# Optimization experiments

Measured on AMD Instinct MI355X. Metric: run time of the kernel, lower is better.

## Reference

```python
import jax, jax.numpy as jnp
import numpy as np

ANNEAL = 0.01
N, D, NUM_CLASSES = 384, 128, 24


def setup_inputs() -> dict:
    key = jax.random.key(0)
    k1, k2 = jax.random.split(key)
    preds = jax.random.normal(k1, (N, D), dtype=jnp.float32)
    # L2-normalize embeddings (standard for SmoothAP cosine similarities)
    preds = preds / jnp.linalg.norm(preds, axis=1, keepdims=True)
    labels = jax.random.randint(k2, (N,), 0, NUM_CLASSES, dtype=jnp.int64)
    return {"preds": preds, "labels": labels}


def reference(preds, labels):
    n = preds.shape[0]
    dt = preds.dtype
    eye = jnp.eye(n, dtype=dt)
    # I_pos[i,j] = 1 iff same label and i != j (lmu.get_all_pairs_indices)
    I_pos = (labels[:, None] == labels[None, :]).astype(dt) * (1 - eye)
    sim = preds @ preds.T                              # [N, N]
    # sim_diff[a,b,c] = sim[a,c] - sim[a,b]  (unsqueeze(1) - unsqueeze(2))
    diff = sim[:, None, :] - sim[:, :, None]           # [N, N, N]
    sg = jax.nn.sigmoid(jnp.clip(diff / ANNEAL, -50.0, 50.0))
    sg = sg * (1 - eye)                                # zero where b == c
    # sum_c sg[a,b,c] * I_pos[a,c], then gate by I_pos[a,b]
    pos_sum = jnp.einsum('abc,ac->ab', sg, I_pos) * I_pos
    sim_pos_rk = 1 + I_pos + pos_sum                   # [N, N]
    sim_all_rk = 1 + jnp.sum(sg, axis=-1)              # [N, N]
    n_pos = jnp.sum(I_pos, axis=1) + 1                 # [N]
    per_i = jnp.sum(sim_pos_rk / sim_all_rk, axis=1) / n_pos
    ap = jnp.sum(jnp.where(n_pos > 1, per_i, jnp.zeros((), dt))) / n
    return (1 - ap)[None]                              # shape (1,), like torch
```

## Files before the change

### kernel.cpp

```cpp
#include <hip/hip_runtime.h>

#define N 384
#define NT 768
#define HALF_ITERS 96

__device__ const float KLOG2E = 144.26950408889634f;

__global__ __launch_bounds__(NT) void smoothap_fused(const float* __restrict__ preds,
                                                     const int* __restrict__ labels,
                                                     float* __restrict__ out) {
    __shared__ __align__(16) float4 s_pa[32];
    __shared__ __align__(16) float2 s_sp[N];
    __shared__ __align__(16) float2 s_part[N];
    __shared__ int   s_lab[N];
    __shared__ float s_red[24];

    const int a = blockIdx.x;
    const int t = threadIdx.x;
    const int half = (t >= N) ? 1 : 0;
    const int b = t - half * N;

    if (t < N) s_lab[t] = labels[t];
    if (t < 32) s_pa[t] = ((const float4*)(preds + (size_t)a * 128))[t];
    __syncthreads();

    if (t < N) {
        const float4* pt = (const float4*)(preds + (size_t)t * 128);
        float acc = 0.f;
#pragma unroll
        for (int k = 0; k < 32; ++k) {
            float4 v = pt[k];
            float4 w = s_pa[k];
            acc = fmaf(v.x, w.x, acc);
            acc = fmaf(v.y, w.y, acc);
            acc = fmaf(v.z, w.z, acc);
            acc = fmaf(v.w, w.w, acc);
        }
        const float posf = (s_lab[t] == s_lab[a] && t != a) ? 1.f : 0.f;
        s_sp[t] = make_float2(acc, posf);
    }
    __syncthreads();

    const float2 me = s_sp[b];
    const float mab = me.x * KLOG2E;
    const float posf = me.y;

    float all_sum = 0.f, pos_sum = 0.f;
    const float4* sp4 = (const float4*)s_sp;
    const int j0 = half * HALF_ITERS;
#pragma unroll 4
    for (int j = j0; j < j0 + HALF_ITERS; ++j) {
        float4 q = sp4[j];
        float e0 = fmaf(q.x, -KLOG2E, mab);
        float sg0 = __builtin_amdgcn_rcpf(1.f + __builtin_amdgcn_exp2f(e0));
        float e1 = fmaf(q.z, -KLOG2E, mab);
        float sg1 = __builtin_amdgcn_rcpf(1.f + __builtin_amdgcn_exp2f(e1));
        all_sum += sg0 + sg1;
        pos_sum = fmaf(sg0, q.y, pos_sum);
        pos_sum = fmaf(sg1, q.w, pos_sum);
    }
    if (half) s_part[b] = make_float2(all_sum, pos_sum);
    __syncthreads();

    float r = 0.f, np = 0.f;
    if (t < N) {
        const float2 o = s_part[b];
        const float all = all_sum + o.x - 0.5f;
        const float pos = pos_sum + o.y - 0.5f * posf;
        r = fmaf(posf, 1.f + pos, 1.f) / (1.f + all);
        np = posf;
    }

    const int lane = t & 63;
    const int wid = t >> 6;
#pragma unroll
    for (int off = 32; off; off >>= 1) {
        r += __shfl_down(r, off);
        np += __shfl_down(np, off);
    }
    if (lane == 0) {
        s_red[wid] = r;
        s_red[12 + wid] = np;
    }
    __syncthreads();
    if (t == 0) {
        float rs = 0.f, ns = 0.f;
#pragma unroll
        for (int w = 0; w < 12; ++w) {
            rs += s_red[w];
            ns += s_red[12 + w];
        }
        const float per_i = (ns > 0.5f) ? rs / (ns + 1.f) : 0.f;
        const float contrib = fmaf(per_i, -1.f / (float)N, (a == 0) ? 1.f : 0.f);
        atomicAdd(out, contrib);
    }
}

extern "C" void kernel_launch(void* const* d_in, const int* in_sizes, int n_in,
                              void* d_out, int out_size, void* d_ws, size_t ws_size,
                              hipStream_t stream) {
    const float* preds = (const float*)d_in[0];
    const int* labels = (const int*)d_in[1];
    float* out = (float*)d_out;

    hipMemsetAsync(out, 0, sizeof(float), stream);
    smoothap_fused<<<N, NT, 0, stream>>>(preds, labels, out);
}
```

Before: 82.74 us.

## Split each anchor row across two blocks of 384 threads

The grid changes from one 768-thread block per anchor to two 384-thread blocks per anchor. Each block handles half of the b indices, and each b is still split over two c-halves inside the block. The point is more, smaller blocks for better scheduling across CUs. The cost is that each anchor's full similarity row (the 384x128 dot products) is now computed twice, and the number of atomic adds doubles.

```diff
diff --git a/kernel.cpp b/kernel.cpp
--- a/kernel.cpp
+++ b/kernel.cpp
@@ -1,8 +1,9 @@
 #include <hip/hip_runtime.h>
 
 #define N 384
-#define NT 768
-#define HALF_ITERS 96
+#define NT 384
+#define HB 192
+#define HJ 96
 
 __device__ const float KLOG2E = 144.26950408889634f;
 
@@ -11,20 +12,19 @@
                                                      float* __restrict__ out) {
     __shared__ __align__(16) float4 s_pa[32];
     __shared__ __align__(16) float2 s_sp[N];
-    __shared__ __align__(16) float2 s_part[N];
+    __shared__ __align__(16) float2 s_part[HB];
     __shared__ int   s_lab[N];
-    __shared__ float s_red[24];
+    __shared__ float s_red[12];
 
-    const int a = blockIdx.x;
+    const int a = blockIdx.x >> 1;
+    const int bh = blockIdx.x & 1;
     const int t = threadIdx.x;
-    const int half = (t >= N) ? 1 : 0;
-    const int b = t - half * N;
 
-    if (t < N) s_lab[t] = labels[t];
+    s_lab[t] = labels[t];
     if (t < 32) s_pa[t] = ((const float4*)(preds + (size_t)a * 128))[t];
     __syncthreads();
 
-    if (t < N) {
+    {
         const float4* pt = (const float4*)(preds + (size_t)t * 128);
         float acc = 0.f;
 #pragma unroll
@@ -36,20 +36,24 @@
             acc = fmaf(v.z, w.z, acc);
             acc = fmaf(v.w, w.w, acc);
         }
-        const float posf = (s_lab[t] == s_lab[a] && t != a) ? 1.f : 0.f;
-        s_sp[t] = make_float2(acc, posf);
+        const float pf = (s_lab[t] == s_lab[a] && t != a) ? 1.f : 0.f;
+        s_sp[t] = make_float2(acc, pf);
     }
     __syncthreads();
 
-    const float2 me = s_sp[b];
-    const float mab = me.x * KLOG2E;
-    const float posf = me.y;
+    const int chalf = (t >= HB) ? 1 : 0;
+    const int b_local = t - chalf * HB;
+    const int b = bh * HB + b_local;
+    const float2 mb = s_sp[b];
+    const float mab = mb.x * KLOG2E;
+    const float posf = mb.y;
+    const float np = s_sp[t].y;
 
     float all_sum = 0.f, pos_sum = 0.f;
     const float4* sp4 = (const float4*)s_sp;
-    const int j0 = half * HALF_ITERS;
+    const int j0 = chalf * HJ;
 #pragma unroll 4
-    for (int j = j0; j < j0 + HALF_ITERS; ++j) {
+    for (int j = j0; j < j0 + HJ; ++j) {
         float4 q = sp4[j];
         float e0 = fmaf(q.x, -KLOG2E, mab);
         float sg0 = __builtin_amdgcn_rcpf(1.f + __builtin_amdgcn_exp2f(e0));
@@ -59,39 +63,39 @@
         pos_sum = fmaf(sg0, q.y, pos_sum);
         pos_sum = fmaf(sg1, q.w, pos_sum);
     }
-    if (half) s_part[b] = make_float2(all_sum, pos_sum);
+    if (chalf) s_part[b_local] = make_float2(all_sum, pos_sum);
     __syncthreads();
 
-    float r = 0.f, np = 0.f;
-    if (t < N) {
-        const float2 o = s_part[b];
+    float r = 0.f;
+    if (t < HB) {
+        const float2 o = s_part[b_local];
         const float all = all_sum + o.x - 0.5f;
         const float pos = pos_sum + o.y - 0.5f * posf;
         r = fmaf(posf, 1.f + pos, 1.f) / (1.f + all);
-        np = posf;
     }
 
     const int lane = t & 63;
     const int wid = t >> 6;
+    float rr = r, nn = np;
 #pragma unroll
     for (int off = 32; off; off >>= 1) {
-        r += __shfl_down(r, off);
-        np += __shfl_down(np, off);
+        rr += __shfl_down(rr, off);
+        nn += __shfl_down(nn, off);
     }
     if (lane == 0) {
-        s_red[wid] = r;
-        s_red[12 + wid] = np;
+        s_red[wid] = rr;
+        s_red[6 + wid] = nn;
     }
     __syncthreads();
     if (t == 0) {
         float rs = 0.f, ns = 0.f;
 #pragma unroll
-        for (int w = 0; w < 12; ++w) {
+        for (int w = 0; w < 6; ++w) {
             rs += s_red[w];
-            ns += s_red[12 + w];
+            ns += s_red[6 + w];
         }
-        const float per_i = (ns > 0.5f) ? rs / (ns + 1.f) : 0.f;
-        const float contrib = fmaf(per_i, -1.f / (float)N, (a == 0) ? 1.f : 0.f);
+        float contrib = (ns > 0.5f) ? -rs / ((ns + 1.f) * (float)N) : 0.f;
+        if (blockIdx.x == 0) contrib += 1.f;
         atomicAdd(out, contrib);
     }
 }
@@ -104,5 +108,5 @@
     float* out = (float*)d_out;
 
     hipMemsetAsync(out, 0, sizeof(float), stream);
-    smoothap_fused<<<N, NT, 0, stream>>>(preds, labels, out);
+    smoothap_fused<<<2 * N, NT, 0, stream>>>(preds, labels, out);
 }
```

After: 87.19 us. 5.4% more time.

## Factor sigmoid into per-element exponentials and compact positives to drop per-pair exp

Applied to the files above, without the earlier changes.

The sigmoid of a scaled similarity difference is rewritten as 1/(1 + A_b*E_c), where A = exp2(k*sim) and E = exp2(-k*sim) are computed once per element. This removes the per-pair exp from the inner loop and leaves one FMA plus one reciprocal per pair. The E values are also compacted with a ballot/popcount prefix so positives come first, which lets the positive sum drop its per-pair multiply and be accumulated only over the leading range. The clamp on each exponent bounds the products, but it differs from clamping the difference itself and could change accuracy for extreme similarities.

```diff
diff --git a/kernel.cpp b/kernel.cpp
--- a/kernel.cpp
+++ b/kernel.cpp
@@ -2,96 +2,141 @@
 
 #define N 384
 #define NT 768
-#define HALF_ITERS 96
+#define HJ 48
 
 __device__ const float KLOG2E = 144.26950408889634f;
+__device__ const float CL = 63.0f;
 
 __global__ __launch_bounds__(NT) void smoothap_fused(const float* __restrict__ preds,
                                                      const int* __restrict__ labels,
                                                      float* __restrict__ out) {
     __shared__ __align__(16) float4 s_pa[32];
-    __shared__ __align__(16) float2 s_sp[N];
+    __shared__ __align__(16) float2 s_AP[N];
+    __shared__ __align__(16) float  s_E[N];
     __shared__ __align__(16) float2 s_part[N];
-    __shared__ int   s_lab[N];
-    __shared__ float s_red[24];
+    __shared__ int   s_wpos[6];
+    __shared__ float s_red[12];
+    __shared__ int   s_P;
 
     const int a = blockIdx.x;
     const int t = threadIdx.x;
-    const int half = (t >= N) ? 1 : 0;
-    const int b = t - half * N;
+    const int lane = t & 63;
+    const int wid = t >> 6;
 
-    if (t < N) s_lab[t] = labels[t];
     if (t < 32) s_pa[t] = ((const float4*)(preds + (size_t)a * 128))[t];
     __syncthreads();
 
+    float posf_t = 0.f, E_t = 0.f;
     if (t < N) {
         const float4* pt = (const float4*)(preds + (size_t)t * 128);
-        float acc = 0.f;
+        float acc0 = 0.f, acc1 = 0.f;
 #pragma unroll
-        for (int k = 0; k < 32; ++k) {
-            float4 v = pt[k];
-            float4 w = s_pa[k];
-            acc = fmaf(v.x, w.x, acc);
-            acc = fmaf(v.y, w.y, acc);
-            acc = fmaf(v.z, w.z, acc);
-            acc = fmaf(v.w, w.w, acc);
+        for (int k = 0; k < 32; k += 2) {
+            float4 v0 = pt[k],     w0 = s_pa[k];
+            float4 v1 = pt[k + 1], w1 = s_pa[k + 1];
+            acc0 = fmaf(v0.x, w0.x, acc0); acc0 = fmaf(v0.y, w0.y, acc0);
+            acc0 = fmaf(v0.z, w0.z, acc0); acc0 = fmaf(v0.w, w0.w, acc0);
+            acc1 = fmaf(v1.x, w1.x, acc1); acc1 = fmaf(v1.y, w1.y, acc1);
+            acc1 = fmaf(v1.z, w1.z, acc1); acc1 = fmaf(v1.w, w1.w, acc1);
         }
-        const float posf = (s_lab[t] == s_lab[a] && t != a) ? 1.f : 0.f;
-        s_sp[t] = make_float2(acc, posf);
+        const float sim = acc0 + acc1;
+        posf_t = (labels[t] == labels[a] && t != a) ? 1.f : 0.f;
+        const float x = fminf(fmaxf(sim * KLOG2E, -CL), CL);
+        const float A_t = __builtin_amdgcn_exp2f(x);
+        E_t = __builtin_amdgcn_exp2f(-x);
+        s_AP[t] = make_float2(A_t, posf_t);
+        unsigned long long m = __ballot(posf_t > 0.5f);
+        if (lane == 0) s_wpos[wid] = __popcll(m);
     }
     __syncthreads();
 
-    const float2 me = s_sp[b];
-    const float mab = me.x * KLOG2E;
-    const float posf = me.y;
+    if (t < N) {
+        int base = 0, P = 0;
+#pragma unroll
+        for (int w = 0; w < 6; ++w) {
+            int c = s_wpos[w];
+            if (w < wid) base += c;
+            P += c;
+        }
+        unsigned long long m = __ballot(posf_t > 0.5f);
+        const int mlt = __popcll(m & ((1ull << lane) - 1ull));
+        const int dest = (posf_t > 0.5f) ? (base + mlt)
+                                         : (P + wid * 64 - base + lane - mlt);
+        s_E[dest] = E_t;
+        if (t == 0) s_P = P;
+    }
+    __syncthreads();
+
+    const int chalf = (t >= N) ? 1 : 0;
+    const int b = t - chalf * N;
+    const float2 ap = s_AP[b];
+    const float A = ap.x;
+    const float posf = ap.y;
+    const int Ps = __builtin_amdgcn_readfirstlane(s_P);
 
     float all_sum = 0.f, pos_sum = 0.f;
-    const float4* sp4 = (const float4*)s_sp;
-    const int j0 = half * HALF_ITERS;
+    const float4* sE4 = (const float4*)s_E;
+    const int jlo = chalf * HJ, jhi = jlo + HJ;
+    const int jPfull = Ps >> 2;
+    const int rem = Ps & 3;
+
+    int j = jlo;
+    const int e1 = (jhi < jPfull) ? jhi : jPfull;
 #pragma unroll 4
-    for (int j = j0; j < j0 + HALF_ITERS; ++j) {
-        float4 q = sp4[j];
-        float e0 = fmaf(q.x, -KLOG2E, mab);
-        float sg0 = __builtin_amdgcn_rcpf(1.f + __builtin_amdgcn_exp2f(e0));
-        float e1 = fmaf(q.z, -KLOG2E, mab);
-        float sg1 = __builtin_amdgcn_rcpf(1.f + __builtin_amdgcn_exp2f(e1));
-        all_sum += sg0 + sg1;
-        pos_sum = fmaf(sg0, q.y, pos_sum);
-        pos_sum = fmaf(sg1, q.w, pos_sum);
+    for (; j < e1; ++j) {
+        float4 q = sE4[j];
+        float s0 = __builtin_amdgcn_rcpf(fmaf(A, q.x, 1.f));
+        float s1 = __builtin_amdgcn_rcpf(fmaf(A, q.y, 1.f));
+        float s2 = __builtin_amdgcn_rcpf(fmaf(A, q.z, 1.f));
+        float s3 = __builtin_amdgcn_rcpf(fmaf(A, q.w, 1.f));
+        const float s = (s0 + s1) + (s2 + s3);
+        all_sum += s;
+        pos_sum += s;
     }
-    if (half) s_part[b] = make_float2(all_sum, pos_sum);
+    if (j == jPfull && j < jhi && rem) {
+        float4 q = sE4[j];
+        const float qv[4] = {q.x, q.y, q.z, q.w};
+#pragma unroll
+        for (int k = 0; k < 4; ++k) {
+            float sg = __builtin_amdgcn_rcpf(fmaf(A, qv[k], 1.f));
+            all_sum += sg;
+            if (k < rem) pos_sum += sg;
+        }
+        ++j;
+    }
+#pragma unroll 4
+    for (; j < jhi; ++j) {
+        float4 q = sE4[j];
+        float s0 = __builtin_amdgcn_rcpf(fmaf(A, q.x, 1.f));
+        float s1 = __builtin_amdgcn_rcpf(fmaf(A, q.y, 1.f));
+        float s2 = __builtin_amdgcn_rcpf(fmaf(A, q.z, 1.f));
+        float s3 = __builtin_amdgcn_rcpf(fmaf(A, q.w, 1.f));
+        all_sum += (s0 + s1) + (s2 + s3);
+    }
+
+    if (chalf) s_part[b] = make_float2(all_sum, pos_sum);
     __syncthreads();
 
-    float r = 0.f, np = 0.f;
+    float r = 0.f;
     if (t < N) {
         const float2 o = s_part[b];
         const float all = all_sum + o.x - 0.5f;
         const float pos = pos_sum + o.y - 0.5f * posf;
-        r = fmaf(posf, 1.f + pos, 1.f) / (1.f + all);
-        np = posf;
+        r = fmaf(posf, 1.f + pos, 1.f) * __builtin_amdgcn_rcpf(1.f + all);
     }
 
-    const int lane = t & 63;
-    const int wid = t >> 6;
+    float rr = r;
 #pragma unroll
-    for (int off = 32; off; off >>= 1) {
-        r += __shfl_down(r, off);
-        np += __shfl_down(np, off);
-    }
-    if (lane == 0) {
-        s_red[wid] = r;
-        s_red[12 + wid] = np;
-    }
+    for (int off = 32; off; off >>= 1) rr += __shfl_down(rr, off);
+    if (lane == 0) s_red[wid] = rr;
     __syncthreads();
     if (t == 0) {
-        float rs = 0.f, ns = 0.f;
+        float rs = 0.f;
 #pragma unroll
-        for (int w = 0; w < 12; ++w) {
-            rs += s_red[w];
-            ns += s_red[12 + w];
-        }
-        const float per_i = (ns > 0.5f) ? rs / (ns + 1.f) : 0.f;
-        const float contrib = fmaf(per_i, -1.f / (float)N, (a == 0) ? 1.f : 0.f);
+        for (int w = 0; w < 12; ++w) rs += s_red[w];
+        const int P = s_P;
+        float contrib = (P > 0) ? (-rs / ((float)(P + 1) * (float)N)) : 0.f;
+        if (a == 0) contrib += 1.f;
         atomicAdd(out, contrib);
     }
 }
```

New measurement: 75.63 us. -8.6%, faster.
